# Optimization experiments

Hardware: AMD Instinct MI355X
Metric: run time of the kernel (lower is better)

Reference implementation:

```python
import jax, jax.numpy as jnp
import numpy as np
from jax import lax

DIM = 384
HEADS = 8
HEAD_DIM = DIM // HEADS
MLP_HIDDEN = int(DIM * 4.0)
B, Hs, Ws = 32, 56, 56
N = Hs * Ws


def layernorm(x, w, b, eps=1e-5):
    mu = jnp.mean(x, axis=-1, keepdims=True)
    var = jnp.mean(jnp.square(x - mu), axis=-1, keepdims=True)
    return (x - mu) * lax.rsqrt(var + eps) * w + b


def setup_inputs() -> dict:
    key = jax.random.key(0)
    ks = jax.random.split(key, 16)
    s = 0.02
    inp = {
        "x": jax.random.normal(ks[0], (B, N, DIM), jnp.float32),
        "H": Hs,
        "W": Ws,
        # CPE depthwise 3x3 conv (groups=dim) -> OIHW kernel [C,1,3,3]
        "cpe_w": jax.random.normal(ks[1], (DIM, 1, 3, 3), jnp.float32) * s,
        "cpe_b": jnp.zeros((DIM,), jnp.float32),
        "ln1_w": jnp.ones((DIM,), jnp.float32),
        "ln1_b": jnp.zeros((DIM,), jnp.float32),
        "qkv_w": jax.random.normal(ks[2], (3 * DIM, DIM), jnp.float32) * s,
        "qkv_b": jnp.zeros((3 * DIM,), jnp.float32),
        "temperature": jnp.ones((HEADS, 1, 1), jnp.float32) * (HEAD_DIM ** -0.5),
        "proj_w": jax.random.normal(ks[3], (DIM, DIM), jnp.float32) * s,
        "proj_b": jnp.zeros((DIM,), jnp.float32),
        "ln2_w": jnp.ones((DIM,), jnp.float32),
        "ln2_b": jnp.zeros((DIM,), jnp.float32),
        "fc1_w": jax.random.normal(ks[4], (MLP_HIDDEN, DIM), jnp.float32) * s,
        "fc1_b": jnp.zeros((MLP_HIDDEN,), jnp.float32),
        "fc2_w": jax.random.normal(ks[5], (DIM, MLP_HIDDEN), jnp.float32) * s,
        "fc2_b": jnp.zeros((DIM,), jnp.float32),
    }
    return inp


def reference(x, H, W, cpe_w, cpe_b, ln1_w, ln1_b, qkv_w, qkv_b, temperature,
              proj_w, proj_b, ln2_w, ln2_b, fc1_w, fc1_b, fc2_w, fc2_b):
    Bn, Nn, C = x.shape
    # --- CPE: depthwise 3x3 conv residual (identity activation, cpe_act=False) ---
    feat = x.transpose(0, 2, 1).reshape(Bn, C, H, W)
    feat = lax.conv_general_dilated(
        feat, cpe_w, window_strides=(1, 1), padding="SAME",
        feature_group_count=C, dimension_numbers=("NCHW", "OIHW", "NCHW"))
    feat = feat + cpe_b[None, :, None, None]
    x = x + feat.reshape(Bn, C, Nn).transpose(0, 2, 1)

    # --- linear attention ---
    cur = layernorm(x, ln1_w, ln1_b)
    qkv = cur @ qkv_w.T + qkv_b                      # [B,N,3C]
    qkv = qkv.reshape(Bn, Nn, 3, HEADS, HEAD_DIM).transpose(2, 0, 3, 1, 4)
    q, k, v = qkv[0], qkv[1], qkv[2]                 # [B,h,N,d]
    q = jax.nn.relu(q)
    k = jax.nn.relu(k)
    k_sum = jnp.sum(k, axis=2)                       # [B,h,d]
    denom = jnp.maximum(jnp.einsum("bhnd,bhd->bhn", q, k_sum)[..., None], 100.0)
    kv = jnp.einsum("bhnd,bhne->bhde", k, v) * temperature  # [B,h,d,d]
    attn_out = jnp.einsum("bhnd,bhde->bhne", q, kv) / denom  # [B,h,N,d]
    attn_out = attn_out.transpose(0, 2, 1, 3).reshape(Bn, Nn, C)
    attn_out = attn_out @ proj_w.T + proj_b
    x = x + attn_out

    # --- MLP residual ---
    cur = layernorm(x, ln2_w, ln2_b)
    h = jax.nn.gelu(cur @ fc1_w.T + fc1_b, approximate=False)
    x = x + (h @ fc2_w.T + fc2_b)
    return x


if __name__ == "__main__":
    out = reference(**setup_inputs())
    print(out.shape, out.dtype)
```

## Files before the change

kernel.cpp:

```cpp
#include <hip/hip_runtime.h>
#include <hip/hip_bf16.h>
#include <math.h>

#define BDIM 384
#define HEADS 8
#define HD 48
#define HID 1536
#define BB 32
#define HH 56
#define WW 56
#define NN 3136
#define MTOT (BB*NN)
#define TPW 8

typedef unsigned short ushort_t;
typedef __attribute__((ext_vector_type(8))) short short8;
typedef __attribute__((ext_vector_type(4))) float floatx4;

__device__ inline float bf2f(ushort_t u){ return __uint_as_float(((unsigned)u)<<16); }
__device__ inline ushort_t f2bf(float f){
  unsigned u = __float_as_uint(f);
  u += 0x7fff + ((u>>16)&1);
  return (ushort_t)(u>>16);
}

__device__ inline float erf_fast(float z){
  float az = fabsf(z);
  float tt = 1.f/(1.f + 0.3275911f*az);
  float poly = tt*(0.254829592f + tt*(-0.284496736f + tt*(1.421413741f +
               tt*(-1.453152027f + tt*1.061405429f))));
  float e = exp2f(-az*az*1.4426950408889634f);
  float r = 1.f - poly*e;
  return copysignf(r, z);
}

__device__ inline void async_ld16(const void* g, void* l){
  __builtin_amdgcn_global_load_lds((const __attribute__((address_space(1))) void*)g,
                                   (__attribute__((address_space(3))) void*)l, 16, 0, 0);
}

__global__ void convert_bf16_kernel(const float* __restrict__ in, ushort_t* __restrict__ out, int n){
  int i = blockIdx.x*256 + threadIdx.x;
  if (i < n) out[i] = f2bf(in[i]);
}

__global__ __launch_bounds__(256)
void cpe_ln1_kernel(const float* __restrict__ x, const float* __restrict__ cw,
                    const float* __restrict__ cb, const float* __restrict__ lw,
                    const float* __restrict__ lb, float* __restrict__ x1out,
                    ushort_t* __restrict__ cur){
  int lane = threadIdx.x & 63, wave = threadIdx.x >> 6;
  size_t base = ((size_t)blockIdx.x*4 + wave) * TPW;
  float wreg[6][9], cbr[6], lwr[6], lbr[6];
  #pragma unroll
  for (int p = 0; p < 6; ++p){
    int c = p*64 + lane;
    cbr[p] = cb[c]; lwr[p] = lw[c]; lbr[p] = lb[c];
    #pragma unroll
    for (int j = 0; j < 9; ++j) wreg[p][j] = cw[c*9+j];
  }
  for (int ti = 0; ti < TPW; ++ti){
    size_t bn = base + ti;
    int b = (int)(bn / NN), n = (int)(bn % NN);
    int h = n / WW, w = n % WW;
    const float* xb = x + ((size_t)b*NN)*BDIM;
    float conv[6];
    #pragma unroll
    for (int p = 0; p < 6; ++p) conv[p] = cbr[p];
    #pragma unroll
    for (int dh = -1; dh <= 1; ++dh){
      int hh = h + dh; if ((unsigned)hh >= HH) continue;
      #pragma unroll
      for (int dw = -1; dw <= 1; ++dw){
        int w2 = w + dw; if ((unsigned)w2 >= WW) continue;
        const float* src = xb + (size_t)(hh*WW + w2)*BDIM + lane;
        int j = (dh+1)*3 + (dw+1);
        #pragma unroll
        for (int p = 0; p < 6; ++p) conv[p] += src[p*64] * wreg[p][j];
      }
    }
    const float* xc = xb + (size_t)n*BDIM + lane;
    float x1[6], s = 0.f, q = 0.f;
    #pragma unroll
    for (int p = 0; p < 6; ++p){
      x1[p] = xc[p*64] + conv[p];
      s += x1[p]; q += x1[p]*x1[p];
    }
    #pragma unroll
    for (int off = 32; off; off >>= 1){
      s += __shfl_xor(s, off);
      q += __shfl_xor(q, off);
    }
    float mean = s*(1.f/384.f);
    float rstd = rsqrtf(q*(1.f/384.f) - mean*mean + 1e-5f);
    float* xo = x1out + bn*BDIM + lane;
    ushort_t* co = cur + bn*BDIM + lane;
    #pragma unroll
    for (int p = 0; p < 6; ++p){
      xo[p*64] = x1[p];
      co[p*64] = f2bf((x1[p]-mean)*rstd*lwr[p] + lbr[p]);
    }
  }
}

__global__ __launch_bounds__(256)
void ln_kernel(const float* __restrict__ xin, const float* __restrict__ lw,
               const float* __restrict__ lb, ushort_t* __restrict__ outb){
  int lane = threadIdx.x & 63, wave = threadIdx.x >> 6;
  size_t base = ((size_t)blockIdx.x*4 + wave) * TPW;
  float lwr[6], lbr[6];
  #pragma unroll
  for (int p = 0; p < 6; ++p){ lwr[p] = lw[p*64+lane]; lbr[p] = lb[p*64+lane]; }
  for (int ti = 0; ti < TPW; ++ti){
    size_t bn = base + ti;
    const float* xi = xin + bn*BDIM + lane;
    float v[6], s = 0.f, q = 0.f;
    #pragma unroll
    for (int p = 0; p < 6; ++p){
      v[p] = xi[p*64];
      s += v[p]; q += v[p]*v[p];
    }
    #pragma unroll
    for (int off = 32; off; off >>= 1){
      s += __shfl_xor(s, off);
      q += __shfl_xor(q, off);
    }
    float mean = s*(1.f/384.f);
    float rstd = rsqrtf(q*(1.f/384.f) - mean*mean + 1e-5f);
    ushort_t* oo = outb + bn*BDIM + lane;
    #pragma unroll
    for (int p = 0; p < 6; ++p) oo[p*64] = f2bf((v[p]-mean)*rstd*lwr[p] + lbr[p]);
  }
}

template<int EP>
__global__ __launch_bounds__(512)
void gemm_kernel(const ushort_t* __restrict__ A, const ushort_t* __restrict__ Bw,
                 const float* __restrict__ bias, const float* __restrict__ resid,
                 void* __restrict__ outp, int Ncols, int K){
  __shared__ __align__(16) ushort_t As[2*256*32];
  __shared__ __align__(16) ushort_t Bs[2*128*32];
  const int t = threadIdx.x;
  const int lane = t & 63, wave = t >> 6;
  const int wm = wave >> 1, wn = wave & 1;

  const int gx = gridDim.x;
  const int nwg = gx * gridDim.y;
  int orig = blockIdx.y * gx + blockIdx.x;
  int qn = nwg >> 3, rn = nwg & 7;
  int xcd = orig & 7, pos = orig >> 3;
  int wg = (xcd < rn ? xcd*(qn+1) : rn*(qn+1) + (xcd-rn)*qn) + pos;
  int bx = wg % gx;
  int by = wg / gx;

  const size_t m0 = (size_t)by * 256;
  const int n0 = bx * 128;
  const int lrow = lane & 15, lk = (lane >> 4) << 3;
  floatx4 zero4 = {0.f, 0.f, 0.f, 0.f};
  floatx4 acc[4][4];
  #pragma unroll
  for (int i = 0; i < 4; ++i)
    #pragma unroll
    for (int j = 0; j < 4; ++j) acc[i][j] = zero4;

  for (int k0 = 0; k0 < K; k0 += 64){
    #pragma unroll
    for (int l = 0; l < 4; ++l){
      int idx = t + l*512;
      int lbase = (l*512 + wave*64) * 8;
      int arow = (idx >> 2) & 255;
      int ako  = (idx >> 10)*32 + (idx & 3)*8;
      async_ld16(&A[(m0 + arow)*K + (k0 + ako)], &As[lbase]);
      if (l < 2){
        int brow = (idx >> 2) & 127;
        int bko  = (idx >> 9)*32 + (idx & 3)*8;
        async_ld16(&Bw[(size_t)(n0 + brow)*K + (k0 + bko)], &Bs[lbase]);
      }
    }
    __syncthreads();
    #pragma unroll
    for (int half = 0; half < 2; ++half){
      const ushort_t* Ah = &As[half*8192];
      const ushort_t* Bh = &Bs[half*4096];
      short8 af[4], bfr[4];
      #pragma unroll
      for (int i = 0; i < 4; ++i) af[i]  = *(const short8*)&Ah[(wm*64 + i*16 + lrow)*32 + lk];
      #pragma unroll
      for (int j = 0; j < 4; ++j) bfr[j] = *(const short8*)&Bh[(wn*64 + j*16 + lrow)*32 + lk];
      #pragma unroll
      for (int i = 0; i < 4; ++i)
        #pragma unroll
        for (int j = 0; j < 4; ++j)
          acc[i][j] = __builtin_amdgcn_mfma_f32_16x16x32_bf16(af[i], bfr[j], acc[i][j], 0, 0, 0);
    }
    __syncthreads();
  }

  const int quad = lane >> 4;
  #pragma unroll
  for (int i = 0; i < 4; ++i){
    #pragma unroll
    for (int j = 0; j < 4; ++j){
      int gn = n0 + wn*64 + j*16 + lrow;
      float bv = bias[gn];
      #pragma unroll
      for (int r = 0; r < 4; ++r){
        size_t gm = m0 + wm*64 + i*16 + quad*4 + r;
        float v = acc[i][j][r] + bv;
        if constexpr (EP == 0){
          if (gn < 768) v = fmaxf(v, 0.f);
          ((ushort_t*)outp)[gm*Ncols + gn] = f2bf(v);
        } else if constexpr (EP == 1){
          v = 0.5f*v*(1.f + erf_fast(v*0.70710678118f));
          ((ushort_t*)outp)[gm*Ncols + gn] = f2bf(v);
        } else {
          ((float*)outp)[gm*Ncols + gn] = v + resid[gm*Ncols + gn];
        }
      }
    }
  }
}

__global__ __launch_bounds__(256)
void kv_mfma_kernel(const ushort_t* __restrict__ qkv, float* __restrict__ kvT_out,
                    float* __restrict__ ksum_out){
  __shared__ __align__(16) ushort_t smem[2*48*72];
  ushort_t* kT = smem;
  ushort_t* vT = smem + 48*72;
  int bh = blockIdx.x, b = bh >> 3, h = bh & 7;
  int chunk = blockIdx.y;
  int t = threadIdx.x, lane = t & 63, wave = t >> 6;
  int lrow = lane & 15, quad = lane >> 4;
  const ushort_t* kb = qkv + (size_t)b*NN*1152 + 384 + h*48;
  const ushort_t* vb = kb + 384;
  floatx4 acc[9];
  #pragma unroll
  for (int i = 0; i < 9; ++i) acc[i] = (floatx4){0.f,0.f,0.f,0.f};
  float ks = 0.f;

  for (int s = 0; s < 7; ++s){
    int n0 = chunk*448 + s*64;
    #pragma unroll
    for (int p = 0; p < 3; ++p){
      int u = t + p*256;
      int arr = u / 384;
      int r = u - arr*384;
      int d8 = r >> 6;
      int nl = r & 63;
      const ushort_t* src = (arr ? vb : kb) + (size_t)(n0 + nl)*1152 + d8*8;
      ushort_t* dst = arr ? vT : kT;
      uint4 val = *(const uint4*)src;
      ushort_t tmp[8];
      *(uint4*)tmp = val;
      #pragma unroll
      for (int j = 0; j < 8; ++j) dst[(d8*8 + j)*72 + nl] = tmp[j];
    }
    __syncthreads();
    if ((wave >> 1) == (s & 1)){
      int kloc = (wave & 1) * 32;
      short8 af[3], bfv[3];
      #pragma unroll
      for (int i = 0; i < 3; ++i) af[i]  = *(const short8*)&kT[(i*16 + lrow)*72 + kloc + quad*8];
      #pragma unroll
      for (int j = 0; j < 3; ++j) bfv[j] = *(const short8*)&vT[(j*16 + lrow)*72 + kloc + quad*8];
      #pragma unroll
      for (int i = 0; i < 3; ++i)
        #pragma unroll
        for (int j = 0; j < 3; ++j)
          acc[i*3+j] = __builtin_amdgcn_mfma_f32_16x16x32_bf16(af[i], bfv[j], acc[i*3+j], 0, 0, 0);
    }
    if (wave == 3 && lane < 48){
      float s2 = 0.f;
      #pragma unroll
      for (int q8 = 0; q8 < 8; ++q8){
        short8 kk = *(const short8*)&kT[lane*72 + q8*8];
        #pragma unroll
        for (int j = 0; j < 8; ++j) s2 += bf2f((ushort_t)kk[j]);
      }
      ks += s2;
    }
    __syncthreads();
  }

  float* F = (float*)smem;
  #define DUMP(W) if (wave == (W)){ _Pragma("unroll") for (int ti = 0; ti < 9; ++ti){ _Pragma("unroll") for (int r = 0; r < 4; ++r){ int d = (ti/3)*16 + quad*4 + r, e = (ti%3)*16 + lrow; F[d*48 + e] = acc[ti][r]; } } }
  #define ADDF(W) if (wave == (W)){ _Pragma("unroll") for (int ti = 0; ti < 9; ++ti){ _Pragma("unroll") for (int r = 0; r < 4; ++r){ int d = (ti/3)*16 + quad*4 + r, e = (ti%3)*16 + lrow; acc[ti][r] += F[d*48 + e]; } } }
  DUMP(1) __syncthreads(); ADDF(0) __syncthreads();
  DUMP(3) __syncthreads(); ADDF(2) __syncthreads();
  DUMP(2) __syncthreads(); ADDF(0) __syncthreads();
  #undef DUMP
  #undef ADDF
  if (wave == 0){
    #pragma unroll
    for (int ti = 0; ti < 9; ++ti){
      #pragma unroll
      for (int r = 0; r < 4; ++r){
        int d = (ti/3)*16 + quad*4 + r, e = (ti%3)*16 + lrow;
        atomicAdd(&kvT_out[(size_t)bh*2304 + e*48 + d], acc[ti][r]);
      }
    }
  }
  if (wave == 3 && lane < 48) atomicAdd(&ksum_out[bh*48 + lane], ks);
}

__global__ __launch_bounds__(256)
void attn_mfma_kernel(const ushort_t* __restrict__ qkv, const float* __restrict__ kvT,
                      const float* __restrict__ ksum, const float* __restrict__ temp,
                      ushort_t* __restrict__ attn_out){
  __shared__ __align__(16) ushort_t Bs[64*72];
  int bh = blockIdx.x, b = bh >> 3, h = bh & 7;
  int t = threadIdx.x, lane = t & 63, wave = t >> 6;
  int lrow = lane & 15, quad = lane >> 4;
  float tf = temp[h];
  for (int u = t; u < 64*72; u += 256){
    int col = u / 72, d = u - col*72;
    float v = 0.f;
    if (d < 48){
      if (col < 48) v = kvT[(size_t)bh*2304 + col*48 + d] * tf;
      else if (col == 48) v = ksum[bh*48 + d];
    }
    Bs[u] = f2bf(v);
  }
  __syncthreads();
  short8 bfv[4][2];
  #pragma unroll
  for (int j = 0; j < 4; ++j)
    #pragma unroll
    for (int s = 0; s < 2; ++s)
      bfv[j][s] = *(const short8*)&Bs[(j*16 + lrow)*72 + s*32 + quad*8];

  const ushort_t* qb = qkv + (size_t)b*NN*1152 + h*48;
  int n0 = blockIdx.y*256 + wave*64;
  floatx4 acc[4][4];
  #pragma unroll
  for (int i = 0; i < 4; ++i)
    #pragma unroll
    for (int j = 0; j < 4; ++j) acc[i][j] = (floatx4){0.f,0.f,0.f,0.f};

  #pragma unroll
  for (int i = 0; i < 4; ++i){
    int nrow = n0 + i*16 + lrow;
    #pragma unroll
    for (int s = 0; s < 2; ++s){
      short8 af = *(const short8*)&qb[(size_t)nrow*1152 + s*32 + quad*8];
      #pragma unroll
      for (int j = 0; j < 4; ++j)
        acc[i][j] = __builtin_amdgcn_mfma_f32_16x16x32_bf16(af, bfv[j][s], acc[i][j], 0, 0, 0);
    }
  }

  ushort_t* ob = attn_out + (size_t)b*NN*BDIM + h*48;
  #pragma unroll
  for (int i = 0; i < 4; ++i){
    #pragma unroll
    for (int r = 0; r < 4; ++r){
      float den = __shfl(acc[i][3][r], quad*16);
      den = fmaxf(den, 100.f);
      int nrow = n0 + i*16 + quad*4 + r;
      if (nrow < NN){
        #pragma unroll
        for (int j = 0; j < 3; ++j)
          ob[(size_t)nrow*BDIM + j*16 + lrow] = f2bf(acc[i][j][r] / den);
      }
    }
  }
}

extern "C" void kernel_launch(void* const* d_in, const int* in_sizes, int n_in,
                              void* d_out, int out_size, void* d_ws, size_t ws_size,
                              hipStream_t stream){
  const float* x     = (const float*)d_in[0];
  const float* cpe_w = (const float*)d_in[3];
  const float* cpe_b = (const float*)d_in[4];
  const float* ln1_w = (const float*)d_in[5];
  const float* ln1_b = (const float*)d_in[6];
  const float* qkv_w = (const float*)d_in[7];
  const float* qkv_b = (const float*)d_in[8];
  const float* temp  = (const float*)d_in[9];
  const float* proj_w= (const float*)d_in[10];
  const float* proj_b= (const float*)d_in[11];
  const float* ln2_w = (const float*)d_in[12];
  const float* ln2_b = (const float*)d_in[13];
  const float* fc1_w = (const float*)d_in[14];
  const float* fc1_b = (const float*)d_in[15];
  const float* fc2_w = (const float*)d_in[16];
  const float* fc2_b = (const float*)d_in[17];
  float* out = (float*)d_out;

  char* ws = (char*)d_ws;
  size_t off = 0;
  auto alloc = [&](size_t bytes) -> void* {
    void* p = ws + off;
    off += (bytes + 255) & ~(size_t)255;
    return p;
  };
  ushort_t* cur  = (ushort_t*)alloc((size_t)MTOT*BDIM*2);
  ushort_t* big  = (ushort_t*)alloc((size_t)MTOT*HID*2);
  float*    kvT  = (float*)   alloc((size_t)BB*HEADS*HD*HD*4);
  float*    ksum = (float*)   alloc((size_t)BB*HEADS*HD*4);
  ushort_t* wq = (ushort_t*)alloc((size_t)3*BDIM*BDIM*2);
  ushort_t* wp = (ushort_t*)alloc((size_t)BDIM*BDIM*2);
  ushort_t* w1 = (ushort_t*)alloc((size_t)HID*BDIM*2);
  ushort_t* w2 = (ushort_t*)alloc((size_t)BDIM*HID*2);

  convert_bf16_kernel<<<(3*BDIM*BDIM + 255)/256, 256, 0, stream>>>(qkv_w, wq, 3*BDIM*BDIM);
  convert_bf16_kernel<<<(BDIM*BDIM + 255)/256, 256, 0, stream>>>(proj_w, wp, BDIM*BDIM);
  convert_bf16_kernel<<<(HID*BDIM + 255)/256, 256, 0, stream>>>(fc1_w, w1, HID*BDIM);
  convert_bf16_kernel<<<(BDIM*HID + 255)/256, 256, 0, stream>>>(fc2_w, w2, BDIM*HID);

  hipMemsetAsync(kvT, 0, (size_t)BB*HEADS*HD*HD*4, stream);
  hipMemsetAsync(ksum, 0, (size_t)BB*HEADS*HD*4, stream);

  cpe_ln1_kernel<<<MTOT/(4*TPW), 256, 0, stream>>>(x, cpe_w, cpe_b, ln1_w, ln1_b, out, cur);
  gemm_kernel<0><<<dim3(9, MTOT/256), 512, 0, stream>>>(cur, wq, qkv_b, nullptr, big, 1152, BDIM);
  kv_mfma_kernel<<<dim3(BB*HEADS, 7), 256, 0, stream>>>(big, kvT, ksum);
  attn_mfma_kernel<<<dim3(BB*HEADS, 13), 256, 0, stream>>>(big, kvT, ksum, temp, cur);
  gemm_kernel<2><<<dim3(3, MTOT/256), 512, 0, stream>>>(cur, wp, proj_b, out, out, BDIM, BDIM);
  ln_kernel<<<MTOT/(4*TPW), 256, 0, stream>>>(out, ln2_w, ln2_b, cur);
  gemm_kernel<1><<<dim3(12, MTOT/256), 512, 0, stream>>>(cur, w1, fc1_b, nullptr, big, HID, BDIM);
  gemm_kernel<2><<<dim3(3, MTOT/256), 512, 0, stream>>>(big, w2, fc2_b, out, out, BDIM, HID);
}
```

Measured before the change: 1.399 ms.

## Stage full-K weight panel in swizzled LDS and stream A fragments from global

The GEMM kernel now loads a whole 128x384 weight panel into XOR-swizzled shared memory per K chunk and reads A fragments directly from global memory into registers, instead of double-staging both A and B tiles through LDS with async loads. Wave tiling changes to 2x4 with 8x2 MFMA accumulators per wave, and K becomes a template parameter. This cuts LDS traffic and the number of barriers per K step. In exchange, A reads become uncoalesced 16-byte global loads that rely on cache, LDS use grows to 96KB which limits occupancy, and the weight load is no longer overlapped with compute.

```diff
diff --git a/kernel.cpp b/kernel.cpp
--- a/kernel.cpp
+++ b/kernel.cpp
@@ -34,11 +34,6 @@
   return copysignf(r, z);
 }
 
-__device__ inline void async_ld16(const void* g, void* l){
-  __builtin_amdgcn_global_load_lds((const __attribute__((address_space(1))) void*)g,
-                                   (__attribute__((address_space(3))) void*)l, 16, 0, 0);
-}
-
 __global__ void convert_bf16_kernel(const float* __restrict__ in, ushort_t* __restrict__ out, int n){
   int i = blockIdx.x*256 + threadIdx.x;
   if (i < n) out[i] = f2bf(in[i]);
@@ -133,16 +128,15 @@
   }
 }
 
-template<int EP>
+template<int EP, int K>
 __global__ __launch_bounds__(512)
 void gemm_kernel(const ushort_t* __restrict__ A, const ushort_t* __restrict__ Bw,
                  const float* __restrict__ bias, const float* __restrict__ resid,
-                 void* __restrict__ outp, int Ncols, int K){
-  __shared__ __align__(16) ushort_t As[2*256*32];
-  __shared__ __align__(16) ushort_t Bs[2*128*32];
+                 void* __restrict__ outp, int Ncols){
+  __shared__ __align__(16) ushort_t Bs[128*384];
   const int t = threadIdx.x;
   const int lane = t & 63, wave = t >> 6;
-  const int wm = wave >> 1, wn = wave & 1;
+  const int wm = wave >> 2, wn = wave & 3;
 
   const int gx = gridDim.x;
   const int nwg = gx * gridDim.y;
@@ -156,56 +150,66 @@
   const size_t m0 = (size_t)by * 256;
   const int n0 = bx * 128;
   const int lrow = lane & 15, lk = (lane >> 4) << 3;
-  floatx4 zero4 = {0.f, 0.f, 0.f, 0.f};
-  floatx4 acc[4][4];
-  #pragma unroll
-  for (int i = 0; i < 4; ++i)
-    #pragma unroll
-    for (int j = 0; j < 4; ++j) acc[i][j] = zero4;
-
-  for (int k0 = 0; k0 < K; k0 += 64){
-    #pragma unroll
-    for (int l = 0; l < 4; ++l){
-      int idx = t + l*512;
-      int lbase = (l*512 + wave*64) * 8;
-      int arow = (idx >> 2) & 255;
-      int ako  = (idx >> 10)*32 + (idx & 3)*8;
-      async_ld16(&A[(m0 + arow)*K + (k0 + ako)], &As[lbase]);
-      if (l < 2){
-        int brow = (idx >> 2) & 127;
-        int bko  = (idx >> 9)*32 + (idx & 3)*8;
-        async_ld16(&Bw[(size_t)(n0 + brow)*K + (k0 + bko)], &Bs[lbase]);
-      }
+  floatx4 acc[8][2];
+  #pragma unroll
+  for (int i = 0; i < 8; ++i)
+    #pragma unroll
+    for (int j = 0; j < 2; ++j) acc[i][j] = (floatx4){0.f,0.f,0.f,0.f};
+
+  const ushort_t* arow[8];
+  #pragma unroll
+  for (int i = 0; i < 8; ++i)
+    arow[i] = A + (m0 + wm*128 + i*16 + lrow)*K + lk;
+
+  constexpr int NC = K / 384;
+  for (int c = 0; c < NC; ++c){
+    if (c) __syncthreads();
+    #pragma unroll
+    for (int i = 0; i < 12; ++i){
+      int g = t + i*512;
+      int row = g / 48;
+      int kg  = g - row*48;
+      uint4 val = *(const uint4*)&Bw[(size_t)(n0 + row)*K + c*384 + kg*8];
+      int boff = row*768 + ((kg*16) ^ ((row&7)<<4));
+      *(uint4*)((char*)Bs + boff) = val;
     }
     __syncthreads();
-    #pragma unroll
-    for (int half = 0; half < 2; ++half){
-      const ushort_t* Ah = &As[half*8192];
-      const ushort_t* Bh = &Bs[half*4096];
-      short8 af[4], bfr[4];
-      #pragma unroll
-      for (int i = 0; i < 4; ++i) af[i]  = *(const short8*)&Ah[(wm*64 + i*16 + lrow)*32 + lk];
-      #pragma unroll
-      for (int j = 0; j < 4; ++j) bfr[j] = *(const short8*)&Bh[(wn*64 + j*16 + lrow)*32 + lk];
-      #pragma unroll
-      for (int i = 0; i < 4; ++i)
-        #pragma unroll
-        for (int j = 0; j < 4; ++j)
-          acc[i][j] = __builtin_amdgcn_mfma_f32_16x16x32_bf16(af[i], bfr[j], acc[i][j], 0, 0, 0);
-    }
-    __syncthreads();
+
+    #pragma unroll 2
+    for (int ks = 0; ks < 6; ++ks){
+      const int kc = ks*64;
+      #pragma unroll
+      for (int h = 0; h < 2; ++h){
+        short8 af[8];
+        #pragma unroll
+        for (int i = 0; i < 8; ++i)
+          af[i] = *(const short8*)&arow[i][c*384 + kc + h*32];
+        short8 bfr[2];
+        #pragma unroll
+        for (int j = 0; j < 2; ++j){
+          int rb = wn*32 + j*16 + lrow;
+          int boff = rb*768 + (((kc + h*32 + lk)*2) ^ ((rb&7)<<4));
+          bfr[j] = *(const short8*)((const char*)Bs + boff);
+        }
+        #pragma unroll
+        for (int i = 0; i < 8; ++i)
+          #pragma unroll
+          for (int j = 0; j < 2; ++j)
+            acc[i][j] = __builtin_amdgcn_mfma_f32_16x16x32_bf16(af[i], bfr[j], acc[i][j], 0, 0, 0);
+      }
+    }
   }
 
   const int quad = lane >> 4;
   #pragma unroll
-  for (int i = 0; i < 4; ++i){
-    #pragma unroll
-    for (int j = 0; j < 4; ++j){
-      int gn = n0 + wn*64 + j*16 + lrow;
+  for (int i = 0; i < 8; ++i){
+    #pragma unroll
+    for (int j = 0; j < 2; ++j){
+      int gn = n0 + wn*32 + j*16 + lrow;
       float bv = bias[gn];
       #pragma unroll
       for (int r = 0; r < 4; ++r){
-        size_t gm = m0 + wm*64 + i*16 + quad*4 + r;
+        size_t gm = m0 + wm*128 + i*16 + quad*4 + r;
         float v = acc[i][j][r] + bv;
         if constexpr (EP == 0){
           if (gn < 768) v = fmaxf(v, 0.f);
@@ -412,11 +416,11 @@
   hipMemsetAsync(ksum, 0, (size_t)BB*HEADS*HD*4, stream);
 
   cpe_ln1_kernel<<<MTOT/(4*TPW), 256, 0, stream>>>(x, cpe_w, cpe_b, ln1_w, ln1_b, out, cur);
-  gemm_kernel<0><<<dim3(9, MTOT/256), 512, 0, stream>>>(cur, wq, qkv_b, nullptr, big, 1152, BDIM);
+  gemm_kernel<0,384><<<dim3(9, MTOT/256), 512, 0, stream>>>(cur, wq, qkv_b, nullptr, big, 1152);
   kv_mfma_kernel<<<dim3(BB*HEADS, 7), 256, 0, stream>>>(big, kvT, ksum);
   attn_mfma_kernel<<<dim3(BB*HEADS, 13), 256, 0, stream>>>(big, kvT, ksum, temp, cur);
-  gemm_kernel<2><<<dim3(3, MTOT/256), 512, 0, stream>>>(cur, wp, proj_b, out, out, BDIM, BDIM);
+  gemm_kernel<2,384><<<dim3(3, MTOT/256), 512, 0, stream>>>(cur, wp, proj_b, out, out, BDIM);
   ln_kernel<<<MTOT/(4*TPW), 256, 0, stream>>>(out, ln2_w, ln2_b, cur);
-  gemm_kernel<1><<<dim3(12, MTOT/256), 512, 0, stream>>>(cur, w1, fc1_b, nullptr, big, HID, BDIM);
-  gemm_kernel<2><<<dim3(3, MTOT/256), 512, 0, stream>>>(big, w2, fc2_b, out, out, BDIM, HID);
-}
+  gemm_kernel<1,384><<<dim3(12, MTOT/256), 512, 0, stream>>>(cur, w1, fc1_b, nullptr, big, HID);
+  gemm_kernel<2,1536><<<dim3(3, MTOT/256), 512, 0, stream>>>(big, w2, fc2_b, out, out, BDIM);
+}
```

New measurement: 2.445 ms. +74.7%, slower.

## Double-buffer GEMM LDS tiles to overlap global loads with MFMA

Applied to the files above, without the earlier changes.

The GEMM main loop now uses ping-pong LDS buffers with 32-wide K steps. The next tile's async global-to-LDS loads are issued right after fragments are read from the current buffer, so they overlap the MFMA work. This removes one of the two barriers per step and hides load latency. In exchange there are more loop iterations with smaller tiles, and correctness relies on the barrier ordering between the two buffers.

```diff
diff --git a/kernel.cpp b/kernel.cpp
--- a/kernel.cpp
+++ b/kernel.cpp
@@ -138,8 +138,10 @@
 void gemm_kernel(const ushort_t* __restrict__ A, const ushort_t* __restrict__ Bw,
                  const float* __restrict__ bias, const float* __restrict__ resid,
                  void* __restrict__ outp, int Ncols, int K){
-  __shared__ __align__(16) ushort_t As[2*256*32];
-  __shared__ __align__(16) ushort_t Bs[2*128*32];
+  __shared__ __align__(16) ushort_t As0[256*32];
+  __shared__ __align__(16) ushort_t As1[256*32];
+  __shared__ __align__(16) ushort_t Bs0[128*32];
+  __shared__ __align__(16) ushort_t Bs1[128*32];
   const int t = threadIdx.x;
   const int lane = t & 63, wave = t >> 6;
   const int wm = wave >> 1, wn = wave & 1;
@@ -156,44 +158,63 @@
   const size_t m0 = (size_t)by * 256;
   const int n0 = bx * 128;
   const int lrow = lane & 15, lk = (lane >> 4) << 3;
-  floatx4 zero4 = {0.f, 0.f, 0.f, 0.f};
   floatx4 acc[4][4];
   #pragma unroll
   for (int i = 0; i < 4; ++i)
     #pragma unroll
-    for (int j = 0; j < 4; ++j) acc[i][j] = zero4;
-
-  for (int k0 = 0; k0 < K; k0 += 64){
-    #pragma unroll
-    for (int l = 0; l < 4; ++l){
-      int idx = t + l*512;
-      int lbase = (l*512 + wave*64) * 8;
-      int arow = (idx >> 2) & 255;
-      int ako  = (idx >> 10)*32 + (idx & 3)*8;
-      async_ld16(&A[(m0 + arow)*K + (k0 + ako)], &As[lbase]);
-      if (l < 2){
-        int brow = (idx >> 2) & 127;
-        int bko  = (idx >> 9)*32 + (idx & 3)*8;
-        async_ld16(&Bw[(size_t)(n0 + brow)*K + (k0 + bko)], &Bs[lbase]);
-      }
-    }
-    __syncthreads();
-    #pragma unroll
-    for (int half = 0; half < 2; ++half){
-      const ushort_t* Ah = &As[half*8192];
-      const ushort_t* Bh = &Bs[half*4096];
+    for (int j = 0; j < 4; ++j) acc[i][j] = (floatx4){0.f,0.f,0.f,0.f};
+
+  const ushort_t* asrc0 = &A[(m0 + (t >> 2))*K + (t & 3)*8];
+  const ushort_t* asrc1 = &A[(m0 + 128 + (t >> 2))*K + (t & 3)*8];
+  const ushort_t* bsrc  = &Bw[(size_t)(n0 + (t >> 2))*K + (t & 3)*8];
+  const int albase0 = (wave*64)*8;
+  const int albase1 = (512 + wave*64)*8;
+  const int blbase  = (wave*64)*8;
+
+  const int nt = K >> 5;
+
+  async_ld16(asrc0, &As0[albase0]);
+  async_ld16(asrc1, &As0[albase1]);
+  async_ld16(bsrc,  &Bs0[blbase]);
+  __syncthreads();
+
+  for (int ts = 0; ts < nt; ts += 2){
+    {
       short8 af[4], bfr[4];
       #pragma unroll
-      for (int i = 0; i < 4; ++i) af[i]  = *(const short8*)&Ah[(wm*64 + i*16 + lrow)*32 + lk];
-      #pragma unroll
-      for (int j = 0; j < 4; ++j) bfr[j] = *(const short8*)&Bh[(wn*64 + j*16 + lrow)*32 + lk];
+      for (int i = 0; i < 4; ++i) af[i]  = *(const short8*)&As0[(wm*64 + i*16 + lrow)*32 + lk];
+      #pragma unroll
+      for (int j = 0; j < 4; ++j) bfr[j] = *(const short8*)&Bs0[(wn*64 + j*16 + lrow)*32 + lk];
+      int ko = (ts + 1) * 32;
+      async_ld16(asrc0 + ko, &As1[albase0]);
+      async_ld16(asrc1 + ko, &As1[albase1]);
+      async_ld16(bsrc  + ko, &Bs1[blbase]);
       #pragma unroll
       for (int i = 0; i < 4; ++i)
         #pragma unroll
         for (int j = 0; j < 4; ++j)
           acc[i][j] = __builtin_amdgcn_mfma_f32_16x16x32_bf16(af[i], bfr[j], acc[i][j], 0, 0, 0);
-    }
-    __syncthreads();
+      __syncthreads();
+    }
+    {
+      short8 af[4], bfr[4];
+      #pragma unroll
+      for (int i = 0; i < 4; ++i) af[i]  = *(const short8*)&As1[(wm*64 + i*16 + lrow)*32 + lk];
+      #pragma unroll
+      for (int j = 0; j < 4; ++j) bfr[j] = *(const short8*)&Bs1[(wn*64 + j*16 + lrow)*32 + lk];
+      if (ts + 2 < nt){
+        int ko = (ts + 2) * 32;
+        async_ld16(asrc0 + ko, &As0[albase0]);
+        async_ld16(asrc1 + ko, &As0[albase1]);
+        async_ld16(bsrc  + ko, &Bs0[blbase]);
+      }
+      #pragma unroll
+      for (int i = 0; i < 4; ++i)
+        #pragma unroll
+        for (int j = 0; j < 4; ++j)
+          acc[i][j] = __builtin_amdgcn_mfma_f32_16x16x32_bf16(af[i], bfr[j], acc[i][j], 0, 0, 0);
+      __syncthreads();
+    }
   }
 
   const int quad = lane >> 4;
```

After: 1.535 ms. 9.7% more time.
